# Kernel tuning notes

Hardware: AMD Instinct MI355X
Metric: run time of the kernel (lower is better)

The kernel has to match this reference:

```python
import jax, jax.numpy as jnp
import numpy as np

N_NODES = 16  # superpixels per sample (gcn1 nodes)


def setup_inputs() -> dict:
    key = jax.random.key(0)
    ks = jax.random.split(key, 10)
    B, Cin, H, W = 32, 64, 112, 112
    Cout, H2, W2 = 128, 56, 56
    E = 64
    inp = {
        "B_for": jax.random.normal(ks[0], (B, Cin, H, W), jnp.float32),
        "B_fon": jax.random.normal(ks[1], (B, Cout, H2, W2), jnp.float32),
        "seg": jax.random.randint(ks[2], (B, H, W), 0, N_NODES, jnp.int32),
        "src": jax.random.randint(ks[3], (B, E), 0, N_NODES, jnp.int32),
        "dst": jax.random.randint(ks[4], (B, E), 0, N_NODES, jnp.int32),
        "conv_w": jax.random.normal(ks[5], (1, Cin), jnp.float32) * 0.1,
        "conv_b": jnp.zeros((1,), jnp.float32),
        "W1": jax.random.normal(ks[6], (4, 32), jnp.float32) * 0.3,
        "b1": jnp.zeros((32,), jnp.float32),
        "W2": jax.random.normal(ks[7], (32, Cout), jnp.float32) * 0.15,
        "b2": jnp.zeros((Cout,), jnp.float32),
        "fc_w": jax.random.normal(ks[8], (1, N_NODES), jnp.float32) * 0.2,
        "fc_b": jnp.zeros((1,), jnp.float32),
    }
    return inp


def _superpixel_features(L, seg):
    # L: [B,1,H,W] intensity; seg: [B,H,W] labels in [0, N_NODES)
    B, _, H, W = L.shape
    ids = (seg + jnp.arange(B, dtype=seg.dtype)[:, None, None] * N_NODES).reshape(-1)
    Lf = L[:, 0].reshape(-1)
    ones = jnp.ones_like(Lf)
    rows = jnp.broadcast_to(jnp.arange(H, dtype=L.dtype)[None, :, None], (B, H, W)).reshape(-1)
    cols = jnp.broadcast_to(jnp.arange(W, dtype=L.dtype)[None, None, :], (B, H, W)).reshape(-1)
    nseg = B * N_NODES
    cnt = jax.ops.segment_sum(ones, ids, num_segments=nseg)
    s_r = jax.ops.segment_sum(rows, ids, num_segments=nseg)
    s_c = jax.ops.segment_sum(cols, ids, num_segments=nseg)
    s_i = jax.ops.segment_sum(Lf, ids, num_segments=nseg)
    cnt_safe = jnp.maximum(cnt, 1.0)
    feats = jnp.stack([s_r / cnt_safe, s_c / cnt_safe, s_i / cnt_safe, cnt], axis=-1)
    feats = feats.reshape(B, N_NODES, 4)
    # normalize mean_intensity and area columns: (x - mean) / (std + 1), unbiased std
    sub = feats[..., 2:]
    mu = sub.mean(axis=1, keepdims=True)
    sd = jnp.std(sub, axis=1, keepdims=True, ddof=1)
    return jnp.concatenate([feats[..., :2], (sub - mu) / (sd + 1.0)], axis=-1)


def _graph_conv(A, nrm, X, Wt, bt):
    # DGL GraphConv, norm='both': D^{-1/2} A D^{-1/2} X W + b
    agg = jnp.einsum('bij,bjf->bif', A, nrm[..., None] * X)
    return nrm[..., None] * agg @ Wt + bt


def reference(B_for, B_fon, seg, src, dst, conv_w, conv_b, W1, b1, W2, b2, fc_w, fc_b):
    B = B_for.shape[0]
    # 1x1 conv -> single-channel intensity map L
    L = jnp.einsum('bchw,oc->bohw', B_for, conv_w) + conv_b[None, :, None, None]
    X = _superpixel_features(L, seg)  # [B, N, 4]
    # symmetric adjacency from edge list
    bidx = jnp.arange(B)[:, None]
    A = jnp.zeros((B, N_NODES, N_NODES), B_for.dtype)
    A = A.at[bidx, src, dst].set(1.0)
    A = A.at[bidx, dst, src].set(1.0)
    nrm = jnp.clip(A.sum(-1), 1.0, None) ** -0.5
    h1 = jax.nn.relu(_graph_conv(A, nrm, X, W1, b1))   # [B, N, 32]
    h2 = jax.nn.relu(_graph_conv(A, nrm, h1, W2, b2))  # [B, N, 128]
    # fc over nodes: Linear(N -> 1) applied to h2.T  => [B, 128]
    G = jnp.einsum('bnf,n->bf', h2, fc_w[0]) + fc_b[0]
    # broadcast-modulate dense CNN features
    return G[:, :, None, None] * B_fon
```

## Files before the change

### kernel.cpp

```cpp
#include <hip/hip_runtime.h>

#define NN 16
constexpr int BB = 32, CIN = 64, HH = 112, WW = 112;
constexpr int HWC = HH * WW;
constexpr int COUT = 128, HW2 = 56 * 56;
constexpr int NE = 64;
constexpr int NQ = HWC / 4;
constexpr int BPI = 13;
constexpr int PF4 = COUT * HW2 / 4;
constexpr int SBPB = 25;

__global__ __launch_bounds__(256) void k_conv_seg(
    const float* __restrict__ Bfor, const int* __restrict__ seg,
    const float* __restrict__ convw, float* __restrict__ part)
{
    __shared__ float w[CIN];
    __shared__ float acc[8][NN][4];
    const int tid = threadIdx.x;
    const int b   = blockIdx.x / BPI;
    const int blk = blockIdx.x % BPI;

    if (tid < CIN) w[tid] = convw[tid];
    for (int i = tid; i < 8 * NN * 4; i += 256) ((float*)acc)[i] = 0.f;
    __syncthreads();

    const float* base = Bfor + (size_t)b * CIN * HWC;
    const int*   segb = seg  + (size_t)b * HWC;
    const int bank = tid & 7;

    for (int q = blk * 256 + tid; q < NQ; q += BPI * 256) {
        const int p = q * 4;
        float4 s = make_float4(0.f, 0.f, 0.f, 0.f);
        #pragma unroll 8
        for (int c = 0; c < CIN; ++c) {
            float4 v = *reinterpret_cast<const float4*>(base + (size_t)c * HWC + p);
            const float wc = w[c];
            s.x = fmaf(v.x, wc, s.x);
            s.y = fmaf(v.y, wc, s.y);
            s.z = fmaf(v.z, wc, s.z);
            s.w = fmaf(v.w, wc, s.w);
        }
        const int4 sg = *reinterpret_cast<const int4*>(segb + p);
        const float row  = (float)(p / WW);
        const float col0 = (float)(p % WW);
        atomicAdd(&acc[bank][sg.x][0], row);
        atomicAdd(&acc[bank][sg.x][1], col0);
        atomicAdd(&acc[bank][sg.x][2], s.x);
        atomicAdd(&acc[bank][sg.x][3], 1.f);
        atomicAdd(&acc[bank][sg.y][0], row);
        atomicAdd(&acc[bank][sg.y][1], col0 + 1.f);
        atomicAdd(&acc[bank][sg.y][2], s.y);
        atomicAdd(&acc[bank][sg.y][3], 1.f);
        atomicAdd(&acc[bank][sg.z][0], row);
        atomicAdd(&acc[bank][sg.z][1], col0 + 2.f);
        atomicAdd(&acc[bank][sg.z][2], s.z);
        atomicAdd(&acc[bank][sg.z][3], 1.f);
        atomicAdd(&acc[bank][sg.w][0], row);
        atomicAdd(&acc[bank][sg.w][1], col0 + 3.f);
        atomicAdd(&acc[bank][sg.w][2], s.w);
        atomicAdd(&acc[bank][sg.w][3], 1.f);
    }
    __syncthreads();

    if (tid < NN * 4) {
        const int node = tid >> 2, st = tid & 3;
        float v = 0.f;
        #pragma unroll
        for (int k = 0; k < 8; ++k) v += acc[k][node][st];
        part[((b * BPI + blk) * NN + node) * 4 + st] = v;
    }
}

__global__ __launch_bounds__(256) void k_graph_scale(
    const float* __restrict__ part, const int* __restrict__ src,
    const int* __restrict__ dst,  const float* __restrict__ convb,
    const float* __restrict__ W1, const float* __restrict__ b1,
    const float* __restrict__ W2, const float* __restrict__ b2,
    const float* __restrict__ fcw, const float* __restrict__ fcb,
    const float* __restrict__ Bfon, float* __restrict__ out)
{
    const int b    = blockIdx.x / SBPB;
    const int blkb = blockIdx.x % SBPB;
    const int tid  = threadIdx.x;

    __shared__ float X[NN][4];
    __shared__ float A[NN][NN];
    __shared__ float nrm[NN];
    __shared__ float h1s[NN][32];
    __shared__ float agg[NN][32];
    __shared__ float Gs[COUT];

    if (tid < NN * 4) {
        const int node = tid >> 2, st = tid & 3;
        float v = 0.f;
        #pragma unroll
        for (int k = 0; k < BPI; ++k) v += part[((b * BPI + k) * NN + node) * 4 + st];
        ((float*)X)[tid] = v;
    }
    for (int i = tid; i < NN * NN; i += 256) ((float*)A)[i] = 0.f;
    __syncthreads();

    if (tid < NN) {
        const float cnt = X[tid][3];
        const float cs  = fmaxf(cnt, 1.f);
        X[tid][0] = X[tid][0] / cs;
        X[tid][1] = X[tid][1] / cs;
        X[tid][2] = (X[tid][2] + cnt * convb[0]) / cs;
    }
    __syncthreads();

    if (tid < 2) {
        const int c = 2 + tid;
        float mu = 0.f;
        for (int i = 0; i < NN; ++i) mu += X[i][c];
        mu *= (1.f / NN);
        float var = 0.f;
        for (int i = 0; i < NN; ++i) { const float d = X[i][c] - mu; var = fmaf(d, d, var); }
        var *= (1.f / (NN - 1));
        const float inv = 1.f / (sqrtf(var) + 1.f);
        for (int i = 0; i < NN; ++i) X[i][c] = (X[i][c] - mu) * inv;
    }
    if (tid >= 64 && tid < 64 + NE) {
        const int e = tid - 64;
        const int s = src[b * NE + e], d = dst[b * NE + e];
        A[s][d] = 1.f;
        A[d][s] = 1.f;
    }
    __syncthreads();

    if (tid < NN) {
        float rs = 0.f;
        for (int j = 0; j < NN; ++j) rs += A[tid][j];
        nrm[tid] = 1.f / sqrtf(fmaxf(rs, 1.f));
    }
    __syncthreads();

    if (tid < NN * 4) {
        const int i = tid >> 2, k = tid & 3;
        float s = 0.f;
        for (int j = 0; j < NN; ++j) s = fmaf(A[i][j] * nrm[j], X[j][k], s);
        agg[i][k] = s;
    }
    __syncthreads();

    for (int t = tid; t < NN * 32; t += 256) {
        const int i = t >> 5, f = t & 31;
        float s = 0.f;
        #pragma unroll
        for (int k = 0; k < 4; ++k) s = fmaf(agg[i][k], W1[k * 32 + f], s);
        h1s[i][f] = fmaxf(fmaf(nrm[i], s, b1[f]), 0.f);
    }
    __syncthreads();

    for (int t = tid; t < NN * 32; t += 256) {
        const int i = t >> 5, k = t & 31;
        float s = 0.f;
        for (int j = 0; j < NN; ++j) s = fmaf(A[i][j] * nrm[j], h1s[j][k], s);
        agg[i][k] = s;
    }
    __syncthreads();

    if (tid < COUT) {
        const int f = tid;
        float g = fcb[0];
        const float bf = b2[f];
        for (int i = 0; i < NN; ++i) {
            float s = 0.f;
            #pragma unroll 8
            for (int k = 0; k < 32; ++k) s = fmaf(agg[i][k], W2[k * COUT + f], s);
            const float h2 = fmaxf(fmaf(nrm[i], s, bf), 0.f);
            g = fmaf(fcw[i], h2, g);
        }
        Gs[f] = g;
    }
    __syncthreads();

    const float4* bf4 = reinterpret_cast<const float4*>(Bfon) + (size_t)b * PF4;
    float4*       ob4 = reinterpret_cast<float4*>(out)        + (size_t)b * PF4;
    for (int t = blkb * 256 + tid; t < PF4; t += SBPB * 256) {
        const float4 v = bf4[t];
        const float  g = Gs[t / (HW2 / 4)];
        ob4[t] = make_float4(v.x * g, v.y * g, v.z * g, v.w * g);
    }
}

extern "C" void kernel_launch(void* const* d_in, const int* in_sizes, int n_in,
                              void* d_out, int out_size, void* d_ws, size_t ws_size,
                              hipStream_t stream)
{
    const float* Bfor  = (const float*)d_in[0];
    const float* Bfon  = (const float*)d_in[1];
    const int*   seg   = (const int*)d_in[2];
    const int*   src   = (const int*)d_in[3];
    const int*   dst   = (const int*)d_in[4];
    const float* convw = (const float*)d_in[5];
    const float* convb = (const float*)d_in[6];
    const float* W1    = (const float*)d_in[7];
    const float* b1    = (const float*)d_in[8];
    const float* W2    = (const float*)d_in[9];
    const float* b2    = (const float*)d_in[10];
    const float* fcw   = (const float*)d_in[11];
    const float* fcb   = (const float*)d_in[12];

    float* part = (float*)d_ws;
    float* out  = (float*)d_out;

    k_conv_seg<<<BB * BPI, 256, 0, stream>>>(Bfor, seg, convw, part);
    k_graph_scale<<<BB * SBPB, 256, 0, stream>>>(part, src, dst, convb,
                                                 W1, b1, W2, b2, fcw, fcb,
                                                 Bfon, out);
}
```

Baseline: 57.73 us.

## Split conv channels across wavefronts with many small blocks; parallelize G over halves

The conv+segment kernel now launches many more blocks (NQ/64 per sample). Each block's four wavefronts each reduce 16 input channels for 64 pixel quads, and the partial sums are combined through shared memory before one wavefront does the atomic segment accumulation. This raises memory-level parallelism and occupancy for the dominant read of B_for. The cost is a much larger partial-sum buffer (BPI=49 per sample) that the second kernel must reduce, and a padded shared accumulator. In the graph kernel, the per-channel G computation is split across all 256 threads by node halves.

```diff
diff --git a/kernel.cpp b/kernel.cpp
--- a/kernel.cpp
+++ b/kernel.cpp
@@ -6,7 +6,8 @@
 constexpr int COUT = 128, HW2 = 56 * 56;
 constexpr int NE = 64;
 constexpr int NQ = HWC / 4;
-constexpr int BPI = 13;
+constexpr int QPB = 64;
+constexpr int BPI = NQ / QPB;
 constexpr int PF4 = COUT * HW2 / 4;
 constexpr int SBPB = 25;
 
@@ -15,50 +16,68 @@
     const float* __restrict__ convw, float* __restrict__ part)
 {
     __shared__ float w[CIN];
-    __shared__ float acc[8][NN][4];
+    __shared__ float ps[4 * QPB * 5];
+    __shared__ float acc[8 * 80];
     const int tid = threadIdx.x;
     const int b   = blockIdx.x / BPI;
     const int blk = blockIdx.x % BPI;
+    const int cg  = tid >> 6;
+    const int l   = tid & 63;
 
     if (tid < CIN) w[tid] = convw[tid];
-    for (int i = tid; i < 8 * NN * 4; i += 256) ((float*)acc)[i] = 0.f;
-    __syncthreads();
-
-    const float* base = Bfor + (size_t)b * CIN * HWC;
-    const int*   segb = seg  + (size_t)b * HWC;
-    const int bank = tid & 7;
-
-    for (int q = blk * 256 + tid; q < NQ; q += BPI * 256) {
-        const int p = q * 4;
-        float4 s = make_float4(0.f, 0.f, 0.f, 0.f);
-        #pragma unroll 8
-        for (int c = 0; c < CIN; ++c) {
-            float4 v = *reinterpret_cast<const float4*>(base + (size_t)c * HWC + p);
-            const float wc = w[c];
-            s.x = fmaf(v.x, wc, s.x);
-            s.y = fmaf(v.y, wc, s.y);
-            s.z = fmaf(v.z, wc, s.z);
-            s.w = fmaf(v.w, wc, s.w);
+    for (int i = tid; i < 8 * 80; i += 256) acc[i] = 0.f;
+    __syncthreads();
+
+    const int q = blk * QPB + l;
+    const int p = q * 4;
+    const float* base = Bfor + (size_t)b * CIN * HWC + (size_t)(cg * 16) * HWC + p;
+
+    float4 s = make_float4(0.f, 0.f, 0.f, 0.f);
+    #pragma unroll
+    for (int cc = 0; cc < 16; ++cc) {
+        const float4 v = *reinterpret_cast<const float4*>(base + (size_t)cc * HWC);
+        const float wc = w[cg * 16 + cc];
+        s.x = fmaf(v.x, wc, s.x);
+        s.y = fmaf(v.y, wc, s.y);
+        s.z = fmaf(v.z, wc, s.z);
+        s.w = fmaf(v.w, wc, s.w);
+    }
+    ps[cg * 320 + l * 5 + 0] = s.x;
+    ps[cg * 320 + l * 5 + 1] = s.y;
+    ps[cg * 320 + l * 5 + 2] = s.z;
+    ps[cg * 320 + l * 5 + 3] = s.w;
+    __syncthreads();
+
+    if (tid < 64) {
+        float r0 = 0.f, r1 = 0.f, r2 = 0.f, r3 = 0.f;
+        #pragma unroll
+        for (int g = 0; g < 4; ++g) {
+            r0 += ps[g * 320 + tid * 5 + 0];
+            r1 += ps[g * 320 + tid * 5 + 1];
+            r2 += ps[g * 320 + tid * 5 + 2];
+            r3 += ps[g * 320 + tid * 5 + 3];
         }
-        const int4 sg = *reinterpret_cast<const int4*>(segb + p);
-        const float row  = (float)(p / WW);
-        const float col0 = (float)(p % WW);
-        atomicAdd(&acc[bank][sg.x][0], row);
-        atomicAdd(&acc[bank][sg.x][1], col0);
-        atomicAdd(&acc[bank][sg.x][2], s.x);
-        atomicAdd(&acc[bank][sg.x][3], 1.f);
-        atomicAdd(&acc[bank][sg.y][0], row);
-        atomicAdd(&acc[bank][sg.y][1], col0 + 1.f);
-        atomicAdd(&acc[bank][sg.y][2], s.y);
-        atomicAdd(&acc[bank][sg.y][3], 1.f);
-        atomicAdd(&acc[bank][sg.z][0], row);
-        atomicAdd(&acc[bank][sg.z][1], col0 + 2.f);
-        atomicAdd(&acc[bank][sg.z][2], s.z);
-        atomicAdd(&acc[bank][sg.z][3], 1.f);
-        atomicAdd(&acc[bank][sg.w][0], row);
-        atomicAdd(&acc[bank][sg.w][1], col0 + 3.f);
-        atomicAdd(&acc[bank][sg.w][2], s.w);
-        atomicAdd(&acc[bank][sg.w][3], 1.f);
+        const int pp = (blk * QPB + tid) * 4;
+        const int4 sg = *reinterpret_cast<const int4*>(seg + (size_t)b * HWC + pp);
+        const float row  = (float)(pp / WW);
+        const float col0 = (float)(pp % WW);
+        const int k = tid & 7;
+        atomicAdd(&acc[k * 80 + sg.x * 5 + 0], row);
+        atomicAdd(&acc[k * 80 + sg.x * 5 + 1], col0);
+        atomicAdd(&acc[k * 80 + sg.x * 5 + 2], r0);
+        atomicAdd(&acc[k * 80 + sg.x * 5 + 3], 1.f);
+        atomicAdd(&acc[k * 80 + sg.y * 5 + 0], row);
+        atomicAdd(&acc[k * 80 + sg.y * 5 + 1], col0 + 1.f);
+        atomicAdd(&acc[k * 80 + sg.y * 5 + 2], r1);
+        atomicAdd(&acc[k * 80 + sg.y * 5 + 3], 1.f);
+        atomicAdd(&acc[k * 80 + sg.z * 5 + 0], row);
+        atomicAdd(&acc[k * 80 + sg.z * 5 + 1], col0 + 2.f);
+        atomicAdd(&acc[k * 80 + sg.z * 5 + 2], r2);
+        atomicAdd(&acc[k * 80 + sg.z * 5 + 3], 1.f);
+        atomicAdd(&acc[k * 80 + sg.w * 5 + 0], row);
+        atomicAdd(&acc[k * 80 + sg.w * 5 + 1], col0 + 3.f);
+        atomicAdd(&acc[k * 80 + sg.w * 5 + 2], r3);
+        atomicAdd(&acc[k * 80 + sg.w * 5 + 3], 1.f);
     }
     __syncthreads();
 
@@ -66,7 +85,7 @@
         const int node = tid >> 2, st = tid & 3;
         float v = 0.f;
         #pragma unroll
-        for (int k = 0; k < 8; ++k) v += acc[k][node][st];
+        for (int k = 0; k < 8; ++k) v += acc[k * 80 + node * 5 + st];
         part[((b * BPI + blk) * NN + node) * 4 + st] = v;
     }
 }
@@ -88,14 +107,14 @@
     __shared__ float nrm[NN];
     __shared__ float h1s[NN][32];
     __shared__ float agg[NN][32];
+    __shared__ float gpart[2][COUT];
     __shared__ float Gs[COUT];
 
-    if (tid < NN * 4) {
+    if (tid < 64) {
         const int node = tid >> 2, st = tid & 3;
         float v = 0.f;
-        #pragma unroll
         for (int k = 0; k < BPI; ++k) v += part[((b * BPI + k) * NN + node) * 4 + st];
-        ((float*)X)[tid] = v;
+        X[node][st] = v;
     }
     for (int i = tid; i < NN * NN; i += 256) ((float*)A)[i] = 0.f;
     __syncthreads();
@@ -160,19 +179,20 @@
     }
     __syncthreads();
 
-    if (tid < COUT) {
-        const int f = tid;
-        float g = fcb[0];
+    {
+        const int f = tid & 127, half = tid >> 7;
+        float g = 0.f;
         const float bf = b2[f];
-        for (int i = 0; i < NN; ++i) {
+        for (int i = half * 8; i < half * 8 + 8; ++i) {
             float s = 0.f;
-            #pragma unroll 8
+            #pragma unroll
             for (int k = 0; k < 32; ++k) s = fmaf(agg[i][k], W2[k * COUT + f], s);
-            const float h2 = fmaxf(fmaf(nrm[i], s, bf), 0.f);
-            g = fmaf(fcw[i], h2, g);
+            g = fmaf(fcw[i], fmaxf(fmaf(nrm[i], s, bf), 0.f), g);
         }
-        Gs[f] = g;
-    }
+        gpart[half][f] = g;
+    }
+    __syncthreads();
+    if (tid < COUT) Gs[tid] = gpart[0][tid] + gpart[1][tid] + fcb[0];
     __syncthreads();
 
     const float4* bf4 = reinterpret_cast<const float4*>(Bfon) + (size_t)b * PF4;
```

After: 48.84 us. 15.4% less time.
